# Performance work log

Measured on AMD Instinct MI355X. Metric: run time of the kernel, lower is better.

## Reference

```python
import jax, jax.numpy as jnp
import numpy as np

B, D, S, E = 32768, 512, 128, 8


def setup_inputs() -> dict:
    key = jax.random.key(0)
    ks = jax.random.split(key, 8)
    x = jax.random.normal(ks[0], (B, D), dtype=jnp.float32)
    y_index = jax.random.randint(ks[1], (B, 1), 0, E, dtype=jnp.int32)
    y_hard = jax.random.uniform(ks[2], (B, E), dtype=jnp.float32)
    z = jax.random.normal(ks[3], (B, 1), dtype=jnp.float32)
    # per-branch 2-layer MLP params, kaiming-ish scaling
    W1 = jax.random.normal(ks[4], (E, D, S), dtype=jnp.float32) / np.sqrt(D)
    b1 = jax.random.normal(ks[5], (E, S), dtype=jnp.float32) * 0.01
    W2 = jax.random.normal(ks[6], (E, S, D), dtype=jnp.float32) / np.sqrt(S)
    b2 = jax.random.normal(ks[7], (E, D), dtype=jnp.float32) * 0.01
    return {"x": x, "y_index": y_index, "y_hard": y_hard, "z": z,
            "W1": W1, "b1": b1, "W2": W2, "b2": b2}


def reference(x, y_index, y_hard, z, W1, b1, W2, b2):
    # out = relu(x); each token b routed to branch y_index[b];
    # branch MLP: relu(out @ W1[e] + b1[e]) @ W2[e] + b2[e], scaled by z, plus residual.
    # y_hard unused (eval path / backward_on_y_hard=False).
    n_branches = W1.shape[0]
    yi = y_index[:, 0]                                   # [B]
    onehot = jax.nn.one_hot(yi, n_branches, dtype=x.dtype)  # [B,E]
    out = jax.nn.relu(x)                                 # [B,D]
    h = jax.nn.relu(jnp.einsum('bd,eds->bes', out, W1) + b1[None])  # [B,E,S]
    h_sel = jnp.einsum('bes,be->bs', h, onehot)          # [B,S] hidden of routed branch
    o = jnp.einsum('bs,esd->bed', h_sel, W2)             # [B,E,D]
    o_sel = jnp.einsum('bed,be->bd', o, onehot) + b2[yi] # [B,D]
    return x + o_sel * z
```

## Files before the change

kernel.cpp:

```cpp
#include <hip/hip_runtime.h>
#include <hip/hip_bf16.h>

#define NB 32768
#define ND 512
#define NS 128
#define NE 8
#define TPE 160

typedef __attribute__((ext_vector_type(8))) short bf16x8;
typedef __attribute__((ext_vector_type(4))) float f32x4;

__device__ __forceinline__ unsigned short f2b(float f) {
  union { __hip_bfloat16 h; unsigned short u; } cv;
  cv.h = __float2bfloat16(f);
  return cv.u;
}

__device__ __forceinline__ bf16x8 relu_cvt8v(float4 a, float4 b) {
  bf16x8 r;
  r[0] = (short)f2b(fmaxf(a.x, 0.f)); r[1] = (short)f2b(fmaxf(a.y, 0.f));
  r[2] = (short)f2b(fmaxf(a.z, 0.f)); r[3] = (short)f2b(fmaxf(a.w, 0.f));
  r[4] = (short)f2b(fmaxf(b.x, 0.f)); r[5] = (short)f2b(fmaxf(b.y, 0.f));
  r[6] = (short)f2b(fmaxf(b.z, 0.f)); r[7] = (short)f2b(fmaxf(b.w, 0.f));
  return r;
}

__device__ __forceinline__ void gload16(const void* gsrc, void* ldst) {
  __builtin_amdgcn_global_load_lds(
      (const __attribute__((address_space(1))) unsigned int*)gsrc,
      (__attribute__((address_space(3))) unsigned int*)ldst, 16, 0, 0);
}

#define BARV7  asm volatile("s_waitcnt vmcnt(7)\n\ts_barrier" ::: "memory")
#define BARV5  asm volatile("s_waitcnt vmcnt(5)\n\ts_barrier" ::: "memory")
#define BARV2  asm volatile("s_waitcnt vmcnt(2)\n\ts_barrier" ::: "memory")
#define BARV0  asm volatile("s_waitcnt vmcnt(0)\n\ts_barrier" ::: "memory")
#define BARL   asm volatile("s_waitcnt lgkmcnt(0)\n\ts_barrier" ::: "memory")
#define BARV2L asm volatile("s_waitcnt vmcnt(2) lgkmcnt(0)\n\ts_barrier" ::: "memory")
#define CFENCE asm volatile("" ::: "memory")

__global__ void zero_counts_k(int* counts) {
  if (threadIdx.x < NE) counts[threadIdx.x] = 0;
}

__global__ void bin_rows_k(const int* __restrict__ yidx, int* __restrict__ counts,
                           int* __restrict__ bucket) {
  __shared__ int lcnt[NE];
  __shared__ int lbase[NE];
  int tid = threadIdx.x;
  if (tid < NE) lcnt[tid] = 0;
  __syncthreads();
  int b = blockIdx.x * blockDim.x + tid;
  int e = yidx[b];
  int pos = atomicAdd(&lcnt[e], 1);
  __syncthreads();
  if (tid < NE) lbase[tid] = atomicAdd(&counts[tid], lcnt[tid]);
  __syncthreads();
  bucket[e * NB + lbase[e] + pos] = b;
}

__global__ void transpose_cvt_k(const float* __restrict__ in,
                                unsigned short* __restrict__ out, int R, int C) {
  __shared__ float lt[32][33];
  int tpm = (R >> 5) * (C >> 5);
  int mat = blockIdx.x / tpm;
  int rem = blockIdx.x % tpm;
  int tcn = C >> 5;
  int tr = rem / tcn, tc = rem % tcn;
  const float* mi = in + (size_t)mat * R * C;
  unsigned short* mo = out + (size_t)mat * R * C;
  int r = threadIdx.x >> 5, c = threadIdx.x & 31;
#pragma unroll
  for (int i = 0; i < 4; ++i) {
    int rr = r + i * 8;
    lt[rr][c] = mi[(size_t)(tr * 32 + rr) * C + tc * 32 + c];
  }
  __syncthreads();
#pragma unroll
  for (int i = 0; i < 4; ++i) {
    int rr = r + i * 8;
    int orow = tc * 32 + rr;
    int d = tr * 32 + c;
    int ocol = (d & ~63) | ((d & 63) ^ ((orow & 7) << 3));
    mo[(size_t)orow * R + ocol] = f2b(lt[c][rr]);
  }
}

#define M1STAGE(c)                                                        \
  do {                                                                    \
    gload16(g0 + (c) * 128, (char*)wt[(c) % 3] + p0 * 16);                \
    gload16(g1 + (c) * 128, (char*)wt[(c) % 3] + p1 * 16);                \
  } while (0)

#define M1_ITER(c)                                                             \
  do {                                                                         \
    if ((c) <= 5) { M1STAGE((c) + 2); }                                        \
    bf16x8 a0 = *(const bf16x8*)(xtb + arow * 1024 +                           \
                                 (((c) * 128 + l4 * 16) ^ arsw));              \
    bf16x8 a1 = *(const bf16x8*)(xtb + arow * 1024 +                           \
                                 (((c) * 128 + 64 + l4 * 16) ^ arsw));         \
    const unsigned short* wb = wt[(c) % 3];                                    \
    __builtin_amdgcn_s_setprio(1);                                             \
    _Pragma("unroll") for (int nt = 0; nt < 2; ++nt) {                         \
      int n = ng * 32 + nt * 16 + l15;                                         \
      int sw = (n & 7) << 3;                                                   \
      bf16x8 b0 = *(const bf16x8*)&wb[n * 64 + ((l4 * 8) ^ sw)];               \
      bf16x8 b1v = *(const bf16x8*)&wb[n * 64 + ((32 + l4 * 8) ^ sw)];         \
      acc[nt] = __builtin_amdgcn_mfma_f32_16x16x32_bf16(a0, b0, acc[nt], 0, 0, 0);  \
      acc[nt] = __builtin_amdgcn_mfma_f32_16x16x32_bf16(a1, b1v, acc[nt], 0, 0, 0); \
    }                                                                          \
    __builtin_amdgcn_s_setprio(0);                                             \
    if ((c) <= 5) { BARV2; } else if ((c) == 6) { BARV0; }                     \
  } while (0)

#define M2STAGE(c)                                                           \
  do {                                                                       \
    gload16(w2e + (c) * 16384 + p0 * 16, (char*)wt[(c) % 3] + p0 * 16);      \
    gload16(w2e + (c) * 16384 + p1 * 16, (char*)wt[(c) % 3] + p1 * 16);      \
  } while (0)

#define M2_ITER(c)                                                            \
  do {                                                                        \
    if ((c) <= 5) { M2STAGE((c) + 2); }                                       \
    float xe0[4];                                                             \
    int d0 = (c) * 64 + ng * 16 + l15;                                        \
    _Pragma("unroll") for (int r = 0; r < 4; ++r)                             \
      xe0[r] = x[(size_t)orow[r] * ND + d0];                                  \
    float bias0 = b2[e * ND + d0];                                            \
    const unsigned short* wb = wt[(c) % 3];                                   \
    f32x4 acc0 = (f32x4){0.f, 0.f, 0.f, 0.f};                                 \
    __builtin_amdgcn_s_setprio(1);                                            \
    _Pragma("unroll") for (int kk = 0; kk < 4; ++kk) {                        \
      int dl0 = ng * 16 + l15;                                                \
      int sw0 = (dl0 & 7) << 3;                                               \
      bf16x8 bv0 = *(const bf16x8*)&wb[dl0 * 128 + ((kk * 32 + l4 * 8) ^ sw0)]; \
      acc0 = __builtin_amdgcn_mfma_f32_16x16x32_bf16(ha[kk], bv0, acc0, 0, 0, 0); \
    }                                                                         \
    __builtin_amdgcn_s_setprio(0);                                            \
    _Pragma("unroll") for (int r = 0; r < 4; ++r) {                           \
      float r0 = xe0[r] + (acc0[r] + bias0) * zr[r];                          \
      float* p0s = valid[r] ? (out + (size_t)orow[r] * ND + d0) : (osink + tid); \
      *p0s = r0;                                                              \
    }                                                                         \
    if ((c) <= 5) { BARV7; } else if ((c) == 6) { BARV5; }                    \
  } while (0)

__launch_bounds__(512, 4)
__global__ void moe_f(const float* __restrict__ x, const float* __restrict__ z,
                      const float* __restrict__ b1, const float* __restrict__ b2,
                      const unsigned short* __restrict__ w1sw,
                      const unsigned short* __restrict__ w2sw,
                      const int* __restrict__ counts, const int* __restrict__ bucket,
                      float* __restrict__ out, float* __restrict__ osink) {
  __shared__ unsigned short wt[3][8192];
  __shared__ unsigned short xt[32][512];
  char* htb = (char*)wt[2];
  char* xtb = (char*)xt;
  int e = blockIdx.x & 7;
  int t = blockIdx.x >> 3;
  int cnt = counts[e];
  if (t * 32 >= cnt) return;
  int tid = threadIdx.x, w = tid >> 6, lane = tid & 63;
  int l15 = lane & 15, l4 = lane >> 4;
  int rg = w >> 2, ng = w & 3;

#pragma unroll
  for (int j = 0; j < 4; ++j) {
    int row = w * 4 + j;
    int pos = t * 32 + row;
    int ps = (pos < cnt) ? pos : (cnt - 1);
    int rid = bucket[e * NB + ps];
    const float* xp = x + (size_t)rid * ND + lane * 8;
    float4 a = *(const float4*)xp;
    float4 b = *(const float4*)(xp + 4);
    bf16x8 v = relu_cvt8v(a, b);
    *(bf16x8*)(xtb + row * 1024 + ((lane * 16) ^ ((row & 7) << 4))) = v;
  }

  const char* w1e = (const char*)w1sw + (size_t)e * NS * ND * 2;
  const char* w2e = (const char*)w2sw + (size_t)e * ND * NS * 2;
  int p0 = tid, p1 = tid + 512;
  const char* g0 = w1e + (p0 >> 3) * 1024 + (p0 & 7) * 16;
  const char* g1 = w1e + (p1 >> 3) * 1024 + (p1 & 7) * 16;

  M1STAGE(0);
  CFENCE;
  M1STAGE(1);
  BARV2L;

  f32x4 acc[2];
  acc[0] = (f32x4){0.f, 0.f, 0.f, 0.f};
  acc[1] = (f32x4){0.f, 0.f, 0.f, 0.f};
  int arow = rg * 16 + l15;
  int arsw = (arow & 7) << 4;

  M1_ITER(0); M1_ITER(1); M1_ITER(2); M1_ITER(3);
  M1_ITER(4); M1_ITER(5); M1_ITER(6); M1_ITER(7);

#pragma unroll
  for (int nt = 0; nt < 2; ++nt) {
    int col = ng * 32 + nt * 16 + l15;
    float bias = b1[e * NS + col];
#pragma unroll
    for (int r = 0; r < 4; ++r) {
      int row = rg * 16 + l4 * 4 + r;
      int off = (row * 256 + col * 2) ^ ((row & 7) << 4);
      *(unsigned short*)(htb + off) = f2b(fmaxf(acc[nt][r] + bias, 0.f));
    }
  }

  int orow[4];
  bool valid[4];
  float zr[4];
#pragma unroll
  for (int r = 0; r < 4; ++r) {
    int pos = t * 32 + rg * 16 + l4 * 4 + r;
    valid[r] = (pos < cnt);
    int ps = valid[r] ? pos : (cnt - 1);
    orow[r] = bucket[e * NB + ps];
    zr[r] = z[orow[r]];
  }

  M2STAGE(0);
  BARL;
  M2STAGE(1);

  bf16x8 ha[4];
#pragma unroll
  for (int kk = 0; kk < 4; ++kk) {
    int row = rg * 16 + l15;
    int off = (row * 256 + (kk * 32 + l4 * 8) * 2) ^ ((row & 7) << 4);
    ha[kk] = *(const bf16x8*)(htb + off);
  }
  BARV2L;

  M2_ITER(0); M2_ITER(1); M2_ITER(2); M2_ITER(3);
  M2_ITER(4); M2_ITER(5); M2_ITER(6); M2_ITER(7);
}

extern "C" void kernel_launch(void* const* d_in, const int* in_sizes, int n_in,
                              void* d_out, int out_size, void* d_ws, size_t ws_size,
                              hipStream_t stream) {
  const float* x = (const float*)d_in[0];
  const int* yidx = (const int*)d_in[1];
  const float* z = (const float*)d_in[3];
  const float* W1 = (const float*)d_in[4];
  const float* b1 = (const float*)d_in[5];
  const float* W2 = (const float*)d_in[6];
  const float* b2 = (const float*)d_in[7];
  float* out = (float*)d_out;

  char* ws = (char*)d_ws;
  int* counts = (int*)ws;
  int* bucket = (int*)(ws + 256);
  size_t off = 256 + (size_t)NE * NB * 4;
  unsigned short* w1sw = (unsigned short*)(ws + off);
  off += (size_t)NE * NS * ND * 2;
  unsigned short* w2sw = (unsigned short*)(ws + off);
  off += (size_t)NE * ND * NS * 2;
  float* osink = (float*)(ws + off);

  zero_counts_k<<<1, 64, 0, stream>>>(counts);
  bin_rows_k<<<NB / 1024, 1024, 0, stream>>>(yidx, counts, bucket);
  transpose_cvt_k<<<NE * (ND / 32) * (NS / 32), 256, 0, stream>>>(W1, w1sw, ND, NS);
  transpose_cvt_k<<<NE * (NS / 32) * (ND / 32), 256, 0, stream>>>(W2, w2sw, NS, ND);
  moe_f<<<NE * TPE, 512, 0, stream>>>(x, z, b1, b2, w1sw, w2sw, counts, bucket,
                                      out, osink);
}
```

Measured before the change: 59.21 us.

## Defer second-GEMM epilogue to end and prefetch first W2 tile during GEMM1

The second GEMM now accumulates all eight output column chunks in registers and does the residual, bias and z scaling, plus the stores, in one epilogue after the loop. The x loads and output stores no longer sit inside the LDS pipeline, so barriers only wait on weight tile loads (vmcnt(2)/vmcnt(0)). The osink dummy-store path is replaced by a predicated store. The first W2 tile load is issued during the last GEMM1 iteration to hide its latency. The cost is 32 extra accumulator registers and x-load latency that is no longer overlapped with MFMA work.

After: 73.53 us. 1.24x slower.

```diff
diff --git a/kernel.cpp b/kernel.cpp
--- a/kernel.cpp
+++ b/kernel.cpp
@@ -31,8 +31,6 @@
       (__attribute__((address_space(3))) unsigned int*)ldst, 16, 0, 0);
 }
 
-#define BARV7  asm volatile("s_waitcnt vmcnt(7)\n\ts_barrier" ::: "memory")
-#define BARV5  asm volatile("s_waitcnt vmcnt(5)\n\ts_barrier" ::: "memory")
 #define BARV2  asm volatile("s_waitcnt vmcnt(2)\n\ts_barrier" ::: "memory")
 #define BARV0  asm volatile("s_waitcnt vmcnt(0)\n\ts_barrier" ::: "memory")
 #define BARL   asm volatile("s_waitcnt lgkmcnt(0)\n\ts_barrier" ::: "memory")
@@ -92,9 +90,16 @@
     gload16(g1 + (c) * 128, (char*)wt[(c) % 3] + p1 * 16);                \
   } while (0)
 
+#define M2STAGE(c)                                                           \
+  do {                                                                       \
+    gload16(w2e + (c) * 16384 + p0 * 16, (char*)wt[(c) % 3] + p0 * 16);      \
+    gload16(w2e + (c) * 16384 + p1 * 16, (char*)wt[(c) % 3] + p1 * 16);      \
+  } while (0)
+
 #define M1_ITER(c)                                                             \
   do {                                                                         \
     if ((c) <= 5) { M1STAGE((c) + 2); }                                        \
+    if ((c) == 7) { M2STAGE(0); }                                               \
     bf16x8 a0 = *(const bf16x8*)(xtb + arow * 1024 +                           \
                                  (((c) * 128 + l4 * 16) ^ arsw));              \
     bf16x8 a1 = *(const bf16x8*)(xtb + arow * 1024 +                           \
@@ -113,36 +118,20 @@
     if ((c) <= 5) { BARV2; } else if ((c) == 6) { BARV0; }                     \
   } while (0)
 
-#define M2STAGE(c)                                                           \
-  do {                                                                       \
-    gload16(w2e + (c) * 16384 + p0 * 16, (char*)wt[(c) % 3] + p0 * 16);      \
-    gload16(w2e + (c) * 16384 + p1 * 16, (char*)wt[(c) % 3] + p1 * 16);      \
-  } while (0)
-
 #define M2_ITER(c)                                                            \
   do {                                                                        \
     if ((c) <= 5) { M2STAGE((c) + 2); }                                       \
-    float xe0[4];                                                             \
-    int d0 = (c) * 64 + ng * 16 + l15;                                        \
-    _Pragma("unroll") for (int r = 0; r < 4; ++r)                             \
-      xe0[r] = x[(size_t)orow[r] * ND + d0];                                  \
-    float bias0 = b2[e * ND + d0];                                            \
     const unsigned short* wb = wt[(c) % 3];                                   \
-    f32x4 acc0 = (f32x4){0.f, 0.f, 0.f, 0.f};                                 \
     __builtin_amdgcn_s_setprio(1);                                            \
     _Pragma("unroll") for (int kk = 0; kk < 4; ++kk) {                        \
       int dl0 = ng * 16 + l15;                                                \
       int sw0 = (dl0 & 7) << 3;                                               \
       bf16x8 bv0 = *(const bf16x8*)&wb[dl0 * 128 + ((kk * 32 + l4 * 8) ^ sw0)]; \
-      acc0 = __builtin_amdgcn_mfma_f32_16x16x32_bf16(ha[kk], bv0, acc0, 0, 0, 0); \
+      acc2[c] = __builtin_amdgcn_mfma_f32_16x16x32_bf16(ha[kk], bv0,          \
+                                                        acc2[c], 0, 0, 0);    \
     }                                                                         \
     __builtin_amdgcn_s_setprio(0);                                            \
-    _Pragma("unroll") for (int r = 0; r < 4; ++r) {                           \
-      float r0 = xe0[r] + (acc0[r] + bias0) * zr[r];                          \
-      float* p0s = valid[r] ? (out + (size_t)orow[r] * ND + d0) : (osink + tid); \
-      *p0s = r0;                                                              \
-    }                                                                         \
-    if ((c) <= 5) { BARV7; } else if ((c) == 6) { BARV5; }                    \
+    if ((c) <= 5) { BARV2; } else if ((c) == 6) { BARV0; }                    \
   } while (0)
 
 __launch_bounds__(512, 4)
@@ -151,7 +140,7 @@
                       const unsigned short* __restrict__ w1sw,
                       const unsigned short* __restrict__ w2sw,
                       const int* __restrict__ counts, const int* __restrict__ bucket,
-                      float* __restrict__ out, float* __restrict__ osink) {
+                      float* __restrict__ out) {
   __shared__ unsigned short wt[3][8192];
   __shared__ unsigned short xt[32][512];
   char* htb = (char*)wt[2];
@@ -221,7 +210,6 @@
     zr[r] = z[orow[r]];
   }
 
-  M2STAGE(0);
   BARL;
   M2STAGE(1);
 
@@ -234,8 +222,25 @@
   }
   BARV2L;
 
+  f32x4 acc2[8];
+#pragma unroll
+  for (int i = 0; i < 8; ++i) acc2[i] = (f32x4){0.f, 0.f, 0.f, 0.f};
+
   M2_ITER(0); M2_ITER(1); M2_ITER(2); M2_ITER(3);
   M2_ITER(4); M2_ITER(5); M2_ITER(6); M2_ITER(7);
+
+#pragma unroll
+  for (int c = 0; c < 8; ++c) {
+    int d0 = c * 64 + ng * 16 + l15;
+    float bias0 = b2[e * ND + d0];
+#pragma unroll
+    for (int r = 0; r < 4; ++r) {
+      if (valid[r]) {
+        size_t o0 = (size_t)orow[r] * ND + d0;
+        out[o0] = x[o0] + (acc2[c][r] + bias0) * zr[r];
+      }
+    }
+  }
 }
 
 extern "C" void kernel_launch(void* const* d_in, const int* in_sizes, int n_in,
@@ -257,13 +262,10 @@
   unsigned short* w1sw = (unsigned short*)(ws + off);
   off += (size_t)NE * NS * ND * 2;
   unsigned short* w2sw = (unsigned short*)(ws + off);
-  off += (size_t)NE * ND * NS * 2;
-  float* osink = (float*)(ws + off);
 
   zero_counts_k<<<1, 64, 0, stream>>>(counts);
   bin_rows_k<<<NB / 1024, 1024, 0, stream>>>(yidx, counts, bucket);
   transpose_cvt_k<<<NE * (ND / 32) * (NS / 32), 256, 0, stream>>>(W1, w1sw, ND, NS);
   transpose_cvt_k<<<NE * (NS / 32) * (ND / 32), 256, 0, stream>>>(W2, w2sw, NS, ND);
-  moe_f<<<NE * TPE, 512, 0, stream>>>(x, z, b1, b2, w1sw, w2sw, counts, bucket,
-                                      out, osink);
-}
+  moe_f<<<NE * TPE, 512, 0, stream>>>(x, z, b1, b2, w1sw, w2sw, counts, bucket, out);
+}
```
